# Kernel tuning notes

Measured on AMD Instinct MI355X. Metric: run time of the kernel, lower is better.

The kernel has to match this reference:

```python
import jax, jax.numpy as jnp
import numpy as np

TOP_K = 2

def setup_inputs() -> dict:
    key = jax.random.key(0)
    k1, k2 = jax.random.split(key)
    G, S, D, E = 4, 2048, 2048, 64
    x = jax.random.normal(k1, (G, S, D), dtype=jnp.float32)
    # xavier_normal-ish scale for the gate kernel
    W = jax.random.normal(k2, (D, E), dtype=jnp.float32) * (2.0 / (D + E)) ** 0.5
    b = jnp.zeros((E,), dtype=jnp.float32)
    return {"x": x, "W": W, "b": b, "expert_capacity": 64}

def reference(x, W, b, expert_capacity):
    # gate projection: [G,S,D] @ [D,E] -> [G,S,E]
    gating_logits = jnp.einsum('gsd,de->gse', x, W) + b
    gating_probs = jax.nn.softmax(gating_logits, axis=-1)
    # top-k experts per token
    expert_gate, expert_index = jax.lax.top_k(gating_probs, TOP_K)  # [G,S,K]
    E = gating_probs.shape[2]
    expert_mask = jax.nn.one_hot(expert_index, E)  # [G,S,K,E]
    # position of each token within its chosen expert (1-based for selected slots)
    position_in_expert = jnp.cumsum(expert_mask, axis=1) * expert_mask  # [G,S,K,E]
    valid_assignment = position_in_expert < expert_capacity
    expert_gate_valid = expert_gate[..., None] * valid_assignment.astype(expert_gate.dtype)
    # one-hot over capacity slots: [G,S,K,E,C]
    combine_per_assignment = expert_gate_valid[..., None] * jax.nn.one_hot(
        position_in_expert, expert_capacity)
    combine_tensor = jnp.sum(combine_per_assignment, axis=2)  # [G,S,E,C]
    combine_tensor = combine_tensor[..., 1:]  # drop position-0 slot -> [G,S,E,C-1]
    dispatch_mask = combine_tensor.astype(bool)
    loss = 0.0  # training=False path
    return combine_tensor, dispatch_mask, loss
```

## Files before the change

### kernel.cpp

```cpp
#include <hip/hip_runtime.h>
#include <cstdint>
#include <cstddef>

#define G_    4
#define S_    2048
#define D_    2048
#define E_    64
#define NTOK  (G_ * S_)
#define CAPM1 63
#define COMBINE_SZ ((size_t)NTOK * E_ * CAPM1)
#define KSLICES 8
#define KCHUNK  (D_ / KSLICES)

__global__ __launch_bounds__(256) void gemm_partial_k(
    const float* __restrict__ x, const float* __restrict__ W,
    float* __restrict__ partial)
{
    __shared__ float xs[16][64];
    __shared__ float wls[16][64];

    const int tid     = threadIdx.x;
    const int tokBase = blockIdx.x * 64;
    const int kBase   = blockIdx.y * KCHUNK;

    const int tt = (tid >> 4) << 2;
    const int ee = (tid & 15) << 2;

    const int xrow = tid >> 2;
    const int xkq  = (tid & 3) << 2;
    const int wkr  = tid >> 4;
    const int wec  = (tid & 15) << 2;

    float acc[4][4];
#pragma unroll
    for (int i = 0; i < 4; ++i)
#pragma unroll
        for (int j = 0; j < 4; ++j) acc[i][j] = 0.f;

    for (int kc = 0; kc < KCHUNK; kc += 16) {
        const float4 xv = *reinterpret_cast<const float4*>(
            &x[(size_t)(tokBase + xrow) * D_ + (size_t)(kBase + kc + xkq)]);
        const float4 wv = *reinterpret_cast<const float4*>(
            &W[(size_t)(kBase + kc + wkr) * E_ + wec]);
        __syncthreads();
        xs[xkq + 0][xrow] = xv.x;
        xs[xkq + 1][xrow] = xv.y;
        xs[xkq + 2][xrow] = xv.z;
        xs[xkq + 3][xrow] = xv.w;
        *reinterpret_cast<float4*>(&wls[wkr][wec]) = wv;
        __syncthreads();
#pragma unroll
        for (int k = 0; k < 16; ++k) {
            const float4 xa = *reinterpret_cast<const float4*>(&xs[k][tt]);
            const float4 wb = *reinterpret_cast<const float4*>(&wls[k][ee]);
            acc[0][0] += xa.x * wb.x; acc[0][1] += xa.x * wb.y;
            acc[0][2] += xa.x * wb.z; acc[0][3] += xa.x * wb.w;
            acc[1][0] += xa.y * wb.x; acc[1][1] += xa.y * wb.y;
            acc[1][2] += xa.y * wb.z; acc[1][3] += xa.y * wb.w;
            acc[2][0] += xa.z * wb.x; acc[2][1] += xa.z * wb.y;
            acc[2][2] += xa.z * wb.z; acc[2][3] += xa.z * wb.w;
            acc[3][0] += xa.w * wb.x; acc[3][1] += xa.w * wb.y;
            acc[3][2] += xa.w * wb.z; acc[3][3] += xa.w * wb.w;
        }
    }

    float* dst = partial + (size_t)blockIdx.y * ((size_t)NTOK * E_);
#pragma unroll
    for (int i = 0; i < 4; ++i) {
        float4 v = make_float4(acc[i][0], acc[i][1], acc[i][2], acc[i][3]);
        *reinterpret_cast<float4*>(&dst[(size_t)(tokBase + tt + i) * E_ + ee]) = v;
    }
}

__global__ __launch_bounds__(256) void softmax_top2_k(
    const float* __restrict__ partial, const float* __restrict__ b,
    int* __restrict__ e1, int* __restrict__ e2,
    float* __restrict__ g1, float* __restrict__ g2)
{
    const int lane = threadIdx.x & 63;
    const int w    = threadIdx.x >> 6;
    const int tok  = blockIdx.x * 4 + w;

    float v = b[lane];
#pragma unroll
    for (int sl = 0; sl < KSLICES; ++sl)
        v += partial[(size_t)sl * NTOK * E_ + (size_t)tok * E_ + lane];

    float m = v;
#pragma unroll
    for (int off = 32; off >= 1; off >>= 1) m = fmaxf(m, __shfl_xor(m, off));
    float p = expf(v - m);
    float s = p;
#pragma unroll
    for (int off = 32; off >= 1; off >>= 1) s += __shfl_xor(s, off);
    p = p / s;

    float bp = p; int bi = lane;
#pragma unroll
    for (int off = 32; off >= 1; off >>= 1) {
        float po = __shfl_xor(bp, off);
        int   io = __shfl_xor(bi, off);
        if (po > bp || (po == bp && io < bi)) { bp = po; bi = io; }
    }
    float p2 = (lane == bi) ? -1.0f : p;
    float bp2 = p2; int bi2 = lane;
#pragma unroll
    for (int off = 32; off >= 1; off >>= 1) {
        float po = __shfl_xor(bp2, off);
        int   io = __shfl_xor(bi2, off);
        if (po > bp2 || (po == bp2 && io < bi2)) { bp2 = po; bi2 = io; }
    }

    if (lane == 0) {
        e1[tok] = bi;  e2[tok] = bi2;
        g1[tok] = bp;  g2[tok] = bp2;
    }
}

__global__ __launch_bounds__(1024) void route_pos_k(
    const int* __restrict__ e1, const int* __restrict__ e2,
    const float* __restrict__ g1, const float* __restrict__ g2,
    int4* __restrict__ recI, float2* __restrict__ recF,
    float* __restrict__ out)
{
    __shared__ int cnt[2][32][64];

    const int g    = blockIdx.x;
    const int lane = threadIdx.x & 63;
    const int wid  = threadIdx.x >> 6;
    const unsigned long long ltmask = ((unsigned long long)1 << lane) - 1;

    int myE[2][2];
    int rank[2][2];

#pragma unroll
    for (int seg = 0; seg < 2; ++seg) {
        const int wseg = seg * 16 + wid;
        const int tok  = g * S_ + wseg * 64 + lane;
        const int ea = e1[tok];
        const int eb = e2[tok];
        myE[seg][0] = ea;
        myE[seg][1] = eb;
#pragma unroll
        for (int k = 0; k < 2; ++k) {
            const int me = k ? eb : ea;
            int r = 0;
            for (int e = 0; e < 64; ++e) {
                unsigned long long mask = __ballot(me == e);
                if (lane == e) cnt[k][wseg][e] = __popcll(mask);
                if (me == e)   r = __popcll(mask & ltmask);
            }
            rank[seg][k] = r;
        }
    }
    __syncthreads();

    if (threadIdx.x < 128) {
        const int k = threadIdx.x >> 6;
        const int e = threadIdx.x & 63;
        int run = 0;
        for (int w = 0; w < 32; ++w) {
            int c = cnt[k][w][e];
            cnt[k][w][e] = run;
            run += c;
        }
    }
    __syncthreads();

#pragma unroll
    for (int seg = 0; seg < 2; ++seg) {
        const int wseg = seg * 16 + wid;
        const int tok  = g * S_ + wseg * 64 + lane;
        int pm1[2];
#pragma unroll
        for (int k = 0; k < 2; ++k) {
            const int e   = myE[seg][k];
            const int pos = cnt[k][wseg][e] + rank[seg][k] + 1;
            pm1[k] = (pos <= CAPM1) ? (pos - 1) : -1;
        }
        recI[tok] = make_int4(myE[seg][0], myE[seg][1], pm1[0], pm1[1]);
        recF[tok] = make_float2(g1[tok], g2[tok]);
    }

    if (g == 0 && threadIdx.x == 0) out[2 * COMBINE_SZ] = 0.0f;
}

__global__ __launch_bounds__(256) void write_all_k(
    const int4* __restrict__ recI, const float2* __restrict__ recF,
    float* __restrict__ out)
{
    const size_t nvec = (2 * COMBINE_SZ) / 4;
    const size_t stride = (size_t)gridDim.x * blockDim.x;

    for (size_t i = (size_t)blockIdx.x * blockDim.x + threadIdx.x;
         i < nvec; i += stride) {
        const size_t f = i * 4;
        const bool isMask = f >= COMBINE_SZ;
        uint32_t fm = (uint32_t)(isMask ? f - COMBINE_SZ : f);

        uint32_t row = (uint32_t)(((uint64_t)fm * 272696337ULL) >> 34);
        uint32_t c   = fm - row * 63u;

        uint32_t e = row & 63u, tok = row >> 6;
        int4   ri = recI[tok];
        float2 rf = recF[tok];
        int c1 = (e == (uint32_t)ri.x) ? ri.z : -1;
        int c2 = (e == (uint32_t)ri.y) ? ri.w : -1;
        float v1 = isMask ? 1.0f : rf.x;
        float v2 = isMask ? 1.0f : rf.y;

        float4 v;
        float* vp = &v.x;
#pragma unroll
        for (int j = 0; j < 4; ++j) {
            if (c == 63u) {
                c = 0; ++row;
                e = row & 63u; tok = row >> 6;
                ri = recI[tok]; rf = recF[tok];
                c1 = (e == (uint32_t)ri.x) ? ri.z : -1;
                c2 = (e == (uint32_t)ri.y) ? ri.w : -1;
                v1 = isMask ? 1.0f : rf.x;
                v2 = isMask ? 1.0f : rf.y;
            }
            vp[j] = ((int)c == c1) ? v1 : ((int)c == c2) ? v2 : 0.0f;
            ++c;
        }
        *reinterpret_cast<float4*>(&out[f]) = v;
    }
}

extern "C" void kernel_launch(void* const* d_in, const int* in_sizes, int n_in,
                              void* d_out, int out_size, void* d_ws, size_t ws_size,
                              hipStream_t stream)
{
    const float* x = (const float*)d_in[0];
    const float* W = (const float*)d_in[1];
    const float* b = (const float*)d_in[2];
    float* out = (float*)d_out;

    float* partial = (float*)d_out;

    int*    e1   = (int*)d_ws;
    int*    e2   = e1 + NTOK;
    float*  g1   = (float*)(e2 + NTOK);
    float*  g2   = g1 + NTOK;
    int4*   recI = (int4*)(g2 + NTOK);
    float2* recF = (float2*)(recI + NTOK);

    gemm_partial_k<<<dim3(NTOK / 64, KSLICES), 256, 0, stream>>>(x, W, partial);
    softmax_top2_k<<<NTOK / 4, 256, 0, stream>>>(partial, b, e1, e2, g1, g2);
    route_pos_k<<<G_, 1024, 0, stream>>>(e1, e2, g1, g2, recI, recF, out);
    write_all_k<<<2048, 256, 0, stream>>>(recI, recF, out);
}
```

Measured before the change: 396.5 us.

## Enlarge GEMM register tiles with prefetch and merge combine/mask writes

The gate GEMM now gives each block 256 tokens and a 32-deep K tile, with each thread computing an 8x8 register tile. The next tile's global loads are prefetched into registers during compute, and the K split doubles to 16 slices. The output writer now handles only the combine tensor and derives the mask value from each computed value, writing both arrays in one pass so the routing record is read once instead of twice. This brings more register pressure and more partial-sum traffic for the softmax kernel to reduce.

After: 397.7 us. Within noise of the previous version (+0.3%).

```diff
diff --git a/kernel.cpp b/kernel.cpp
--- a/kernel.cpp
+++ b/kernel.cpp
@@ -9,66 +9,107 @@
 #define NTOK  (G_ * S_)
 #define CAPM1 63
 #define COMBINE_SZ ((size_t)NTOK * E_ * CAPM1)
-#define KSLICES 8
+#define KSLICES 16
 #define KCHUNK  (D_ / KSLICES)
+#define KT      32
+#define NTILES  (KCHUNK / KT)
+#define XPAD    260
 
 __global__ __launch_bounds__(256) void gemm_partial_k(
     const float* __restrict__ x, const float* __restrict__ W,
     float* __restrict__ partial)
 {
-    __shared__ float xs[16][64];
-    __shared__ float wls[16][64];
+    __shared__ float xs[KT][XPAD];
+    __shared__ float wls[KT][64];
 
     const int tid     = threadIdx.x;
-    const int tokBase = blockIdx.x * 64;
+    const int tokBase = blockIdx.x * 256;
     const int kBase   = blockIdx.y * KCHUNK;
 
-    const int tt = (tid >> 4) << 2;
-    const int ee = (tid & 15) << 2;
-
-    const int xrow = tid >> 2;
-    const int xkq  = (tid & 3) << 2;
-    const int wkr  = tid >> 4;
-    const int wec  = (tid & 15) << 2;
-
-    float acc[4][4];
-#pragma unroll
-    for (int i = 0; i < 4; ++i)
-#pragma unroll
-        for (int j = 0; j < 4; ++j) acc[i][j] = 0.f;
-
-    for (int kc = 0; kc < KCHUNK; kc += 16) {
-        const float4 xv = *reinterpret_cast<const float4*>(
-            &x[(size_t)(tokBase + xrow) * D_ + (size_t)(kBase + kc + xkq)]);
-        const float4 wv = *reinterpret_cast<const float4*>(
-            &W[(size_t)(kBase + kc + wkr) * E_ + wec]);
+    const int tt = (tid >> 3) * 8;
+    const int ee = (tid & 7) * 8;
+
+    const int xrow = tid >> 3;
+    const int k4   = (tid & 7) * 4;
+
+    float acc[8][8];
+#pragma unroll
+    for (int i = 0; i < 8; ++i)
+#pragma unroll
+        for (int j = 0; j < 8; ++j) acc[i][j] = 0.f;
+
+    float4 xv[8];
+    float4 wv[2];
+
+#pragma unroll
+    for (int r = 0; r < 8; ++r)
+        xv[r] = *reinterpret_cast<const float4*>(
+            &x[(size_t)(tokBase + xrow + r * 32) * D_ + (size_t)(kBase + k4)]);
+#pragma unroll
+    for (int wi = 0; wi < 2; ++wi) {
+        const int idx = tid + wi * 256;
+        wv[wi] = *reinterpret_cast<const float4*>(
+            &W[(size_t)(kBase + (idx >> 4)) * E_ + (idx & 15) * 4]);
+    }
+
+    for (int t = 0; t < NTILES; ++t) {
         __syncthreads();
-        xs[xkq + 0][xrow] = xv.x;
-        xs[xkq + 1][xrow] = xv.y;
-        xs[xkq + 2][xrow] = xv.z;
-        xs[xkq + 3][xrow] = xv.w;
-        *reinterpret_cast<float4*>(&wls[wkr][wec]) = wv;
+#pragma unroll
+        for (int r = 0; r < 8; ++r) {
+            const int ltok = xrow + r * 32;
+            xs[k4 + 0][ltok] = xv[r].x;
+            xs[k4 + 1][ltok] = xv[r].y;
+            xs[k4 + 2][ltok] = xv[r].z;
+            xs[k4 + 3][ltok] = xv[r].w;
+        }
+#pragma unroll
+        for (int wi = 0; wi < 2; ++wi) {
+            const int idx = tid + wi * 256;
+            *reinterpret_cast<float4*>(&wls[idx >> 4][(idx & 15) * 4]) = wv[wi];
+        }
         __syncthreads();
-#pragma unroll
-        for (int k = 0; k < 16; ++k) {
-            const float4 xa = *reinterpret_cast<const float4*>(&xs[k][tt]);
-            const float4 wb = *reinterpret_cast<const float4*>(&wls[k][ee]);
-            acc[0][0] += xa.x * wb.x; acc[0][1] += xa.x * wb.y;
-            acc[0][2] += xa.x * wb.z; acc[0][3] += xa.x * wb.w;
-            acc[1][0] += xa.y * wb.x; acc[1][1] += xa.y * wb.y;
-            acc[1][2] += xa.y * wb.z; acc[1][3] += xa.y * wb.w;
-            acc[2][0] += xa.z * wb.x; acc[2][1] += xa.z * wb.y;
-            acc[2][2] += xa.z * wb.z; acc[2][3] += xa.z * wb.w;
-            acc[3][0] += xa.w * wb.x; acc[3][1] += xa.w * wb.y;
-            acc[3][2] += xa.w * wb.z; acc[3][3] += xa.w * wb.w;
+
+        if (t + 1 < NTILES) {
+            const int kt = kBase + (t + 1) * KT;
+#pragma unroll
+            for (int r = 0; r < 8; ++r)
+                xv[r] = *reinterpret_cast<const float4*>(
+                    &x[(size_t)(tokBase + xrow + r * 32) * D_ + (size_t)(kt + k4)]);
+#pragma unroll
+            for (int wi = 0; wi < 2; ++wi) {
+                const int idx = tid + wi * 256;
+                wv[wi] = *reinterpret_cast<const float4*>(
+                    &W[(size_t)(kt + (idx >> 4)) * E_ + (idx & 15) * 4]);
+            }
+        }
+
+#pragma unroll 8
+        for (int k = 0; k < KT; ++k) {
+            const float4 a0 = *reinterpret_cast<const float4*>(&xs[k][tt]);
+            const float4 a1 = *reinterpret_cast<const float4*>(&xs[k][tt + 4]);
+            const float4 b0 = *reinterpret_cast<const float4*>(&wls[k][ee]);
+            const float4 b1 = *reinterpret_cast<const float4*>(&wls[k][ee + 4]);
+            float A[8], B[8];
+            A[0]=a0.x; A[1]=a0.y; A[2]=a0.z; A[3]=a0.w;
+            A[4]=a1.x; A[5]=a1.y; A[6]=a1.z; A[7]=a1.w;
+            B[0]=b0.x; B[1]=b0.y; B[2]=b0.z; B[3]=b0.w;
+            B[4]=b1.x; B[5]=b1.y; B[6]=b1.z; B[7]=b1.w;
+#pragma unroll
+            for (int i = 0; i < 8; ++i)
+#pragma unroll
+                for (int j = 0; j < 8; ++j)
+                    acc[i][j] += A[i] * B[j];
         }
     }
 
     float* dst = partial + (size_t)blockIdx.y * ((size_t)NTOK * E_);
 #pragma unroll
-    for (int i = 0; i < 4; ++i) {
-        float4 v = make_float4(acc[i][0], acc[i][1], acc[i][2], acc[i][3]);
-        *reinterpret_cast<float4*>(&dst[(size_t)(tokBase + tt + i) * E_ + ee]) = v;
+    for (int i = 0; i < 8; ++i) {
+        const size_t row = (size_t)(tokBase + tt + i) * E_;
+        *reinterpret_cast<float4*>(&dst[row + ee])     =
+            make_float4(acc[i][0], acc[i][1], acc[i][2], acc[i][3]);
+        *reinterpret_cast<float4*>(&dst[row + ee + 4]) =
+            make_float4(acc[i][4], acc[i][5], acc[i][6], acc[i][7]);
     }
 }
 
@@ -189,14 +230,13 @@
     const int4* __restrict__ recI, const float2* __restrict__ recF,
     float* __restrict__ out)
 {
-    const size_t nvec = (2 * COMBINE_SZ) / 4;
+    const size_t nvec = COMBINE_SZ / 4;
     const size_t stride = (size_t)gridDim.x * blockDim.x;
 
     for (size_t i = (size_t)blockIdx.x * blockDim.x + threadIdx.x;
          i < nvec; i += stride) {
         const size_t f = i * 4;
-        const bool isMask = f >= COMBINE_SZ;
-        uint32_t fm = (uint32_t)(isMask ? f - COMBINE_SZ : f);
+        const uint32_t fm = (uint32_t)f;
 
         uint32_t row = (uint32_t)(((uint64_t)fm * 272696337ULL) >> 34);
         uint32_t c   = fm - row * 63u;
@@ -206,8 +246,6 @@
         float2 rf = recF[tok];
         int c1 = (e == (uint32_t)ri.x) ? ri.z : -1;
         int c2 = (e == (uint32_t)ri.y) ? ri.w : -1;
-        float v1 = isMask ? 1.0f : rf.x;
-        float v2 = isMask ? 1.0f : rf.y;
 
         float4 v;
         float* vp = &v.x;
@@ -219,13 +257,17 @@
                 ri = recI[tok]; rf = recF[tok];
                 c1 = (e == (uint32_t)ri.x) ? ri.z : -1;
                 c2 = (e == (uint32_t)ri.y) ? ri.w : -1;
-                v1 = isMask ? 1.0f : rf.x;
-                v2 = isMask ? 1.0f : rf.y;
             }
-            vp[j] = ((int)c == c1) ? v1 : ((int)c == c2) ? v2 : 0.0f;
+            vp[j] = ((int)c == c1) ? rf.x : ((int)c == c2) ? rf.y : 0.0f;
             ++c;
         }
+        float4 mk;
+        mk.x = (v.x != 0.0f) ? 1.0f : 0.0f;
+        mk.y = (v.y != 0.0f) ? 1.0f : 0.0f;
+        mk.z = (v.z != 0.0f) ? 1.0f : 0.0f;
+        mk.w = (v.w != 0.0f) ? 1.0f : 0.0f;
         *reinterpret_cast<float4*>(&out[f]) = v;
+        *reinterpret_cast<float4*>(&out[f + COMBINE_SZ]) = mk;
     }
 }
 
@@ -247,7 +289,7 @@
     int4*   recI = (int4*)(g2 + NTOK);
     float2* recF = (float2*)(recI + NTOK);
 
-    gemm_partial_k<<<dim3(NTOK / 64, KSLICES), 256, 0, stream>>>(x, W, partial);
+    gemm_partial_k<<<dim3(NTOK / 256, KSLICES), 256, 0, stream>>>(x, W, partial);
     softmax_top2_k<<<NTOK / 4, 256, 0, stream>>>(partial, b, e1, e2, g1, g2);
     route_pos_k<<<G_, 1024, 0, stream>>>(e1, e2, g1, g2, recI, recF, out);
     write_all_k<<<2048, 256, 0, stream>>>(recI, recF, out);
```
